# Kernel optimization log

Hardware: AMD Instinct MI355X
Metric: run time of the kernel (lower is better)

## Reference

```python
import jax, jax.numpy as jnp
import numpy as np

KROT = 8
DIM = 4096
GROUP = 128
N = 16384  # tokens (batch*seq)


def setup_inputs() -> dict:
    key = jax.random.key(0)
    k1, k2, k3 = jax.random.split(key, 3)
    x = jax.random.normal(k1, (N, DIM), dtype=jnp.float16)
    theta = (jax.random.normal(k2, (KROT, DIM // 2)) * 0.5).astype(jnp.float16)
    # pairs: per rotation layer, a permutation of [0, GROUP) tiled across groups
    # (matches torch.randperm(group_size).repeat(num_groups) in the module).
    rng = np.random.default_rng(0)
    single = np.stack([rng.permutation(GROUP) for _ in range(KROT)]).astype(np.int32)  # (KROT, GROUP)
    pairs = jnp.asarray(np.tile(single, (1, DIM // GROUP)))  # (KROT, DIM)
    channel_scales = jax.random.uniform(k3, (1, DIM), minval=0.5, maxval=1.5).astype(jnp.float16)
    return {"x": x, "pairs": pairs, "theta": theta,
            "channel_scales": channel_scales, "group_size": GROUP}


def reference(x, pairs, theta, channel_scales, group_size):
    """Pairwise Givens rotations + per-channel scaling.

    For each rotation layer k, channels are grouped into blocks of
    `group_size`; consecutive entries (pairs[k, 2i], pairs[k, 2i+1]) within a
    group define a rotated channel pair with angle theta[k, i].
    """
    krot, dim = pairs.shape
    # global channel index = group offset + within-group index from `pairs`
    offs = (jnp.arange(dim) // group_size) * group_size            # (dim,)
    gidx = pairs + offs[None, :]                                   # (krot, dim)
    a_idx = gidx[:, 0::2]                                          # (krot, dim//2)
    b_idx = gidx[:, 1::2]                                          # (krot, dim//2)

    for k in range(krot):  # krot is a small fixed constant (8)
        t = theta[k].astype(jnp.float32)
        c = jnp.cos(t).astype(x.dtype)                             # (dim//2,)
        s = jnp.sin(t).astype(x.dtype)
        xa = x[:, a_idx[k]]                                        # (N, dim//2)
        xb = x[:, b_idx[k]]
        x = x.at[:, a_idx[k]].set(c * xa - s * xb)
        x = x.at[:, b_idx[k]].set(s * xa + c * xb)
    return x * channel_scales
```

## Files before the change

### kernel.cpp

```cpp
#include <hip/hip_runtime.h>
#include <hip/hip_fp16.h>


typedef unsigned int uint32;

#define DIM    4096
#define GROUP  128
#define KROT   8
#define NGROUP 32
#define TPAD   (GROUP + 1)

__device__ __forceinline__ float bf16_to_f(unsigned short u) {
    union { uint32 i; float f; } v; v.i = ((uint32)u) << 16; return v.f;
}
__device__ __forceinline__ unsigned short f_to_bf16(float f) {
    union { float f; uint32 i; } v; v.f = f;
    uint32 x = v.i;
    return (unsigned short)((x + 0x7fffu + ((x >> 16) & 1u)) >> 16);
}
__device__ __forceinline__ float fp16_to_f(unsigned short u) {
    __half h = __ushort_as_half(u); return __half2float(h);
}
__device__ __forceinline__ unsigned short f_to_fp16(float f) {
    return __half_as_ushort(__float2half_rn(f));
}
__device__ __forceinline__ float bcast_f(float x, int lane) {
    return __uint_as_float(__builtin_amdgcn_readlane(__float_as_uint(x), lane));
}

__global__ __launch_bounds__(256) void detect_dtype(const uint32* __restrict__ scw,
                                                    int* __restrict__ flag) {
    __shared__ int cbf[256], cfp16[256];
    int b = 0, h = 0;
    for (int i = threadIdx.x; i < 2048; i += 256) {
        uint32 lo = scw[i] & 0xffffu;
        b += (lo >= 0x3F00u && lo <= 0x3FC0u);
        h += (lo >= 0x3800u && lo <= 0x3E00u);
    }
    cbf[threadIdx.x] = b; cfp16[threadIdx.x] = h;
    __syncthreads();
    for (int s = 128; s > 0; s >>= 1) {
        if (threadIdx.x < s) { cbf[threadIdx.x] += cbf[threadIdx.x + s];
                               cfp16[threadIdx.x] += cfp16[threadIdx.x + s]; }
        __syncthreads();
    }
    if (threadIdx.x == 0)
        *flag = (cbf[0] > 1024) ? 1 : ((cfp16[0] > 1024) ? 2 : 0);
}

__global__ __launch_bounds__(256) void rotate_direct(
    const void* __restrict__ Xv,
    const int*  __restrict__ pairs,
    const void* __restrict__ thetav,
    const void* __restrict__ scalesv,
    void* __restrict__ Outv,
    const int* __restrict__ flagp, int defflag)
{
    __shared__ float tile[64][TPAD];
    __shared__ float scl[GROUP];
    const int g    = blockIdx.x;
    const int row0 = blockIdx.y * 64;
    const int tid  = threadIdx.x;
    const int dt   = flagp ? *flagp : defflag;
    const int l    = tid & 63;
    const int w    = tid >> 6;
    const int pmine = w * 16 + (l & 15);

    if (tid < GROUP) {
        int c = g * GROUP + tid;
        scl[tid] = (dt == 1) ? bf16_to_f(((const unsigned short*)scalesv)[c])
                 : (dt == 2) ? fp16_to_f(((const unsigned short*)scalesv)[c])
                 : ((const float*)scalesv)[c];
    }

    int A[KROT], B[KROT]; float C[KROT], S[KROT];
    #pragma unroll
    for (int k = 0; k < KROT; ++k) {
        A[k] = pairs[k * DIM + g * GROUP + 2 * pmine];
        B[k] = pairs[k * DIM + g * GROUP + 2 * pmine + 1];
        int ti = k * (DIM / 2) + g * (GROUP / 2) + pmine;
        float th = (dt == 1) ? bf16_to_f(((const unsigned short*)thetav)[ti])
                 : (dt == 2) ? fp16_to_f(((const unsigned short*)thetav)[ti])
                 : ((const float*)thetav)[ti];
        C[k] = __builtin_cosf(th);
        S[k] = __builtin_sinf(th);
    }

    if (dt == 0) {
        const float4* X4 = (const float4*)Xv;
        for (int i = tid; i < 64 * 32; i += 256) {
            int r = i >> 5, c4 = i & 31;
            float4 v = X4[(size_t)(row0 + r) * (DIM / 4) + g * (GROUP / 4) + c4];
            tile[r][c4 * 4 + 0] = v.x; tile[r][c4 * 4 + 1] = v.y;
            tile[r][c4 * 4 + 2] = v.z; tile[r][c4 * 4 + 3] = v.w;
        }
    } else {
        const uint4* X4 = (const uint4*)Xv;
        for (int i = tid; i < 64 * 16; i += 256) {
            int r = i >> 4, c8 = i & 15;
            uint4 wv = X4[(size_t)(row0 + r) * (DIM / 8) + g * (GROUP / 8) + c8];
            uint32 ws[4] = { wv.x, wv.y, wv.z, wv.w };
            #pragma unroll
            for (int h2 = 0; h2 < 4; ++h2) {
                unsigned short lo = (unsigned short)(ws[h2] & 0xffffu);
                unsigned short hi = (unsigned short)(ws[h2] >> 16);
                tile[r][c8 * 8 + 2 * h2]     = (dt == 1) ? bf16_to_f(lo) : fp16_to_f(lo);
                tile[r][c8 * 8 + 2 * h2 + 1] = (dt == 1) ? bf16_to_f(hi) : fp16_to_f(hi);
            }
        }
    }
    __syncthreads();

    #pragma unroll
    for (int k = 0; k < KROT; ++k) {
        #pragma unroll
        for (int pp = 0; pp < 16; ++pp) {
            int   a = __builtin_amdgcn_readlane(A[k], pp);
            int   b = __builtin_amdgcn_readlane(B[k], pp);
            float c = bcast_f(C[k], pp);
            float s = bcast_f(S[k], pp);
            float xa = tile[l][a], xb = tile[l][b];
            tile[l][a] = c * xa - s * xb;
            tile[l][b] = s * xa + c * xb;
        }
        __syncthreads();
    }

    if (dt == 0) {
        float4* O4 = (float4*)Outv;
        for (int i = tid; i < 64 * 32; i += 256) {
            int r = i >> 5, c4 = i & 31;
            float4 v;
            v.x = tile[r][c4 * 4 + 0] * scl[c4 * 4 + 0];
            v.y = tile[r][c4 * 4 + 1] * scl[c4 * 4 + 1];
            v.z = tile[r][c4 * 4 + 2] * scl[c4 * 4 + 2];
            v.w = tile[r][c4 * 4 + 3] * scl[c4 * 4 + 3];
            O4[(size_t)(row0 + r) * (DIM / 4) + g * (GROUP / 4) + c4] = v;
        }
    } else {
        uint4* O4 = (uint4*)Outv;
        for (int i = tid; i < 64 * 16; i += 256) {
            int r = i >> 4, c8 = i & 15;
            uint32 ws[4];
            #pragma unroll
            for (int h2 = 0; h2 < 4; ++h2) {
                float lo = tile[r][c8 * 8 + 2 * h2]     * scl[c8 * 8 + 2 * h2];
                float hi = tile[r][c8 * 8 + 2 * h2 + 1] * scl[c8 * 8 + 2 * h2 + 1];
                unsigned short ulo = (dt == 1) ? f_to_bf16(lo) : f_to_fp16(lo);
                unsigned short uhi = (dt == 1) ? f_to_bf16(hi) : f_to_fp16(hi);
                ws[h2] = (uint32)ulo | ((uint32)uhi << 16);
            }
            uint4 wv; wv.x = ws[0]; wv.y = ws[1]; wv.z = ws[2]; wv.w = ws[3];
            O4[(size_t)(row0 + r) * (DIM / 8) + g * (GROUP / 8) + c8] = wv;
        }
    }
}

extern "C" void kernel_launch(void* const* d_in, const int* in_sizes, int n_in,
                              void* d_out, int out_size, void* d_ws, size_t ws_size,
                              hipStream_t stream) {
    const void* x      = d_in[0];
    const int*  pairs  = (const int*)d_in[1];
    const void* theta  = d_in[2];
    const void* scales = d_in[3];

    const int N = in_sizes[0] / DIM;
    const int nrowtiles = N / 64;

    int* flag = nullptr;
    if (d_ws != nullptr && ws_size >= sizeof(int)) {
        flag = (int*)d_ws;
        detect_dtype<<<1, 256, 0, stream>>>((const uint32*)scales, flag);
    }
    rotate_direct<<<dim3(NGROUP, nrowtiles), 256, 0, stream>>>(
        x, pairs, theta, scales, d_out, flag, 0);
}
```

Measured before the change: 481.3 us.

## Compose rotations into per-group matrices and apply via MFMA GEMM

Adds a kernel that folds the eight Givens rotation layers and the channel scaling into one dense 128x128 matrix per channel group, stored in the workspace. A second kernel then multiplies each 64-row input tile by that matrix with fp16/bf16 MFMA instructions, using XOR-swizzled LDS, in place of the serial per-pair LDS read-modify-write loop. This trades a few extra FLOPs and a matrix-composition prologue for much shorter dependent LDS chains. Rounding changes because the rotations are fused and the composed matrix is stored in half precision. The new path only runs when the workspace is large enough.

```diff
diff --git a/kernel.cpp b/kernel.cpp
--- a/kernel.cpp
+++ b/kernel.cpp
@@ -3,6 +3,7 @@
 
 
 typedef unsigned int uint32;
+typedef unsigned short ushort;
 
 #define DIM    4096
 #define GROUP  128
@@ -10,18 +11,22 @@
 #define NGROUP 32
 #define TPAD   (GROUP + 1)
 
-__device__ __forceinline__ float bf16_to_f(unsigned short u) {
+typedef float    f32x4 __attribute__((ext_vector_type(4)));
+typedef _Float16 f16x8 __attribute__((ext_vector_type(8)));
+typedef short    s16x8 __attribute__((ext_vector_type(8)));
+
+__device__ __forceinline__ float bf16_to_f(ushort u) {
     union { uint32 i; float f; } v; v.i = ((uint32)u) << 16; return v.f;
 }
-__device__ __forceinline__ unsigned short f_to_bf16(float f) {
+__device__ __forceinline__ ushort f_to_bf16(float f) {
     union { float f; uint32 i; } v; v.f = f;
     uint32 x = v.i;
-    return (unsigned short)((x + 0x7fffu + ((x >> 16) & 1u)) >> 16);
-}
-__device__ __forceinline__ float fp16_to_f(unsigned short u) {
+    return (ushort)((x + 0x7fffu + ((x >> 16) & 1u)) >> 16);
+}
+__device__ __forceinline__ float fp16_to_f(ushort u) {
     __half h = __ushort_as_half(u); return __half2float(h);
 }
-__device__ __forceinline__ unsigned short f_to_fp16(float f) {
+__device__ __forceinline__ ushort f_to_fp16(float f) {
     return __half_as_ushort(__float2half_rn(f));
 }
 __device__ __forceinline__ float bcast_f(float x, int lane) {
@@ -46,6 +51,237 @@
     }
     if (threadIdx.x == 0)
         *flag = (cbf[0] > 1024) ? 1 : ((cfp16[0] > 1024) ? 2 : 0);
+}
+
+__global__ __launch_bounds__(256) void compose_M(
+    const int*  __restrict__ pairs,
+    const void* __restrict__ thetav,
+    const void* __restrict__ scalesv,
+    ushort*     __restrict__ Mt,
+    const int*  __restrict__ flagp)
+{
+    __shared__ float tile[64][TPAD];
+    const int dt = *flagp;
+    if (dt == 0) return;
+    const int g    = blockIdx.x >> 1;
+    const int half = blockIdx.x & 1;
+    const int r0   = half * 64;
+    const int tid  = threadIdx.x;
+    const int l    = tid & 63;
+    const int w    = tid >> 6;
+    const int pmine = w * 16 + (l & 15);
+
+    int A[KROT], B[KROT]; float C[KROT], S[KROT];
+    #pragma unroll
+    for (int k = 0; k < KROT; ++k) {
+        A[k] = pairs[k * DIM + g * GROUP + 2 * pmine];
+        B[k] = pairs[k * DIM + g * GROUP + 2 * pmine + 1];
+        int ti = k * (DIM / 2) + g * (GROUP / 2) + pmine;
+        float th = (dt == 1) ? bf16_to_f(((const ushort*)thetav)[ti])
+                             : fp16_to_f(((const ushort*)thetav)[ti]);
+        float c = __builtin_cosf(th), s = __builtin_sinf(th);
+        if (dt == 1) { c = bf16_to_f(f_to_bf16(c)); s = bf16_to_f(f_to_bf16(s)); }
+        else         { c = fp16_to_f(f_to_fp16(c)); s = fp16_to_f(f_to_fp16(s)); }
+        C[k] = c; S[k] = s;
+    }
+
+    for (int idx = tid; idx < 64 * GROUP; idx += 256) {
+        int r = idx >> 7, c = idx & 127;
+        tile[r][c] = (r0 + r == c) ? 1.0f : 0.0f;
+    }
+    __syncthreads();
+
+    #pragma unroll
+    for (int k = 0; k < KROT; ++k) {
+        #pragma unroll
+        for (int pp = 0; pp < 16; ++pp) {
+            int   a = __builtin_amdgcn_readlane(A[k], pp);
+            int   b = __builtin_amdgcn_readlane(B[k], pp);
+            float c = bcast_f(C[k], pp);
+            float s = bcast_f(S[k], pp);
+            float xa = tile[l][a], xb = tile[l][b];
+            tile[l][a] = c * xa - s * xb;
+            tile[l][b] = s * xa + c * xb;
+        }
+        __syncthreads();
+    }
+
+    for (int it = 0; it < 4; ++it) {
+        int idx = it * 256 + tid;
+        int j = idx >> 3, cc = idx & 7;
+        float sj = (dt == 1) ? bf16_to_f(((const ushort*)scalesv)[g * GROUP + j])
+                             : fp16_to_f(((const ushort*)scalesv)[g * GROUP + j]);
+        uint32 ws4[4];
+        #pragma unroll
+        for (int h2 = 0; h2 < 4; ++h2) {
+            float lo = tile[cc * 8 + 2 * h2][j]     * sj;
+            float hi = tile[cc * 8 + 2 * h2 + 1][j] * sj;
+            ushort ulo = (dt == 1) ? f_to_bf16(lo) : f_to_fp16(lo);
+            ushort uhi = (dt == 1) ? f_to_bf16(hi) : f_to_fp16(hi);
+            ws4[h2] = (uint32)ulo | ((uint32)uhi << 16);
+        }
+        uint4 v; v.x = ws4[0]; v.y = ws4[1]; v.z = ws4[2]; v.w = ws4[3];
+        *(uint4*)(Mt + (size_t)g * GROUP * GROUP + (size_t)j * GROUP
+                     + ((size_t)(half * 8 + cc)) * 8) = v;
+    }
+}
+
+template <int DT>
+__device__ __forceinline__ void gemm_core(const ushort* __restrict__ xs,
+                                          const ushort* __restrict__ mt,
+                                          f32x4 acc[2][4], int l, int wr, int wc)
+{
+    const int lr = l & 15, q = l >> 4;
+    union U { uint4 u; f16x8 h; s16x8 s; };
+    #pragma unroll
+    for (int kk = 0; kk < 4; ++kk) {
+        U av[2];
+        #pragma unroll
+        for (int mf = 0; mf < 2; ++mf) {
+            int r = wr * 32 + mf * 16 + lr;
+            int c = (kk * 4 + q) ^ (r & 7);
+            av[mf].u = *(const uint4*)(xs + (size_t)r * GROUP + (size_t)c * 8);
+        }
+        #pragma unroll
+        for (int nf = 0; nf < 4; ++nf) {
+            int n = wc * 64 + nf * 16 + lr;
+            int c = (kk * 4 + q) ^ (n & 7);
+            U bv; bv.u = *(const uint4*)(mt + (size_t)n * GROUP + (size_t)c * 8);
+            #pragma unroll
+            for (int mf = 0; mf < 2; ++mf) {
+                if constexpr (DT == 2)
+                    acc[mf][nf] = __builtin_amdgcn_mfma_f32_16x16x32_f16(
+                        av[mf].h, bv.h, acc[mf][nf], 0, 0, 0);
+                else
+                    acc[mf][nf] = __builtin_amdgcn_mfma_f32_16x16x32_bf16(
+                        av[mf].s, bv.s, acc[mf][nf], 0, 0, 0);
+            }
+        }
+    }
+}
+
+__global__ __launch_bounds__(256) void rotate_gemm(
+    const void* __restrict__ Xv,
+    const ushort* __restrict__ Mt,
+    void* __restrict__ Outv,
+    const int* __restrict__ flagp,
+    const int* __restrict__ pairs,
+    const void* __restrict__ thetav,
+    const void* __restrict__ scalesv)
+{
+    __shared__ union __align__(16) {
+        struct { ushort xs[64 * GROUP]; ushort mt[GROUP * GROUP]; } s;
+        ushort os[64][136];
+        struct { float tile[64][TPAD]; float scl[GROUP]; } fb;
+    } sh;
+    const int dt   = *flagp;
+    const int row0 = blockIdx.x * 64;
+    const int g    = blockIdx.y;
+    const int tid  = threadIdx.x;
+    const int l    = tid & 63;
+    const int w    = tid >> 6;
+
+    if (dt != 0) {
+        const uint4* X4 = (const uint4*)Xv;
+        #pragma unroll
+        for (int it = 0; it < 4; ++it) {
+            int i = it * 256 + tid;
+            int r = i >> 4, c = i & 15;
+            uint4 v = X4[(size_t)(row0 + r) * (DIM / 8) + g * (GROUP / 8) + c];
+            *(uint4*)(sh.s.xs + (size_t)r * GROUP + (size_t)(c ^ (r & 7)) * 8) = v;
+        }
+        const uint4* M4 = (const uint4*)(Mt + (size_t)g * GROUP * GROUP);
+        #pragma unroll
+        for (int it = 0; it < 8; ++it) {
+            int i = it * 256 + tid;
+            int n = i >> 4, c = i & 15;
+            uint4 v = M4[i];
+            *(uint4*)(sh.s.mt + (size_t)n * GROUP + (size_t)(c ^ (n & 7)) * 8) = v;
+        }
+        __syncthreads();
+
+        const int wr = w >> 1, wc = w & 1;
+        f32x4 acc[2][4];
+        #pragma unroll
+        for (int mf = 0; mf < 2; ++mf)
+            #pragma unroll
+            for (int nf = 0; nf < 4; ++nf)
+                acc[mf][nf] = (f32x4)0.0f;
+
+        if (dt == 2) gemm_core<2>(sh.s.xs, sh.s.mt, acc, l, wr, wc);
+        else         gemm_core<1>(sh.s.xs, sh.s.mt, acc, l, wr, wc);
+        __syncthreads();
+
+        const int lr = l & 15, q = l >> 4;
+        #pragma unroll
+        for (int mf = 0; mf < 2; ++mf) {
+            #pragma unroll
+            for (int nf = 0; nf < 4; ++nf) {
+                int r  = wr * 32 + mf * 16 + q * 4;
+                int cc = wc * 64 + nf * 16 + lr;
+                #pragma unroll
+                for (int j = 0; j < 4; ++j) {
+                    float vv = acc[mf][nf][j];
+                    sh.os[r + j][cc] = (dt == 1) ? f_to_bf16(vv) : f_to_fp16(vv);
+                }
+            }
+        }
+        __syncthreads();
+
+        uint4* O4 = (uint4*)Outv;
+        #pragma unroll
+        for (int it = 0; it < 2; ++it) {
+            int i = it * 256 + tid;
+            int r = i >> 3, c8 = i & 7;
+            uint4 v = *(const uint4*)(&sh.os[r][c8 * 8]);
+            O4[(size_t)(row0 + r) * (DIM / 8) + g * (GROUP / 8) + c8] = v;
+        }
+        return;
+    }
+
+    const int pmine = w * 16 + (l & 15);
+    if (tid < GROUP) sh.fb.scl[tid] = ((const float*)scalesv)[g * GROUP + tid];
+    int A[KROT], B[KROT]; float C[KROT], S[KROT];
+    #pragma unroll
+    for (int k = 0; k < KROT; ++k) {
+        A[k] = pairs[k * DIM + g * GROUP + 2 * pmine];
+        B[k] = pairs[k * DIM + g * GROUP + 2 * pmine + 1];
+        int ti = k * (DIM / 2) + g * (GROUP / 2) + pmine;
+        float th = ((const float*)thetav)[ti];
+        C[k] = __builtin_cosf(th); S[k] = __builtin_sinf(th);
+    }
+    const float4* Xf = (const float4*)Xv;
+    for (int i = tid; i < 64 * 32; i += 256) {
+        int r = i >> 5, c4 = i & 31;
+        float4 v = Xf[(size_t)(row0 + r) * (DIM / 4) + g * (GROUP / 4) + c4];
+        sh.fb.tile[r][c4 * 4 + 0] = v.x; sh.fb.tile[r][c4 * 4 + 1] = v.y;
+        sh.fb.tile[r][c4 * 4 + 2] = v.z; sh.fb.tile[r][c4 * 4 + 3] = v.w;
+    }
+    __syncthreads();
+    #pragma unroll
+    for (int k = 0; k < KROT; ++k) {
+        #pragma unroll
+        for (int pp = 0; pp < 16; ++pp) {
+            int   a = __builtin_amdgcn_readlane(A[k], pp);
+            int   b = __builtin_amdgcn_readlane(B[k], pp);
+            float c = bcast_f(C[k], pp);
+            float s = bcast_f(S[k], pp);
+            float xa = sh.fb.tile[l][a], xb = sh.fb.tile[l][b];
+            sh.fb.tile[l][a] = c * xa - s * xb;
+            sh.fb.tile[l][b] = s * xa + c * xb;
+        }
+        __syncthreads();
+    }
+    float4* Of = (float4*)Outv;
+    for (int i = tid; i < 64 * 32; i += 256) {
+        int r = i >> 5, c4 = i & 31;
+        float4 v;
+        v.x = sh.fb.tile[r][c4 * 4 + 0] * sh.fb.scl[c4 * 4 + 0];
+        v.y = sh.fb.tile[r][c4 * 4 + 1] * sh.fb.scl[c4 * 4 + 1];
+        v.z = sh.fb.tile[r][c4 * 4 + 2] * sh.fb.scl[c4 * 4 + 2];
+        v.w = sh.fb.tile[r][c4 * 4 + 3] * sh.fb.scl[c4 * 4 + 3];
+        Of[(size_t)(row0 + r) * (DIM / 4) + g * (GROUP / 4) + c4] = v;
+    }
 }
 
 __global__ __launch_bounds__(256) void rotate_direct(
@@ -68,24 +304,22 @@
 
     if (tid < GROUP) {
         int c = g * GROUP + tid;
-        scl[tid] = (dt == 1) ? bf16_to_f(((const unsigned short*)scalesv)[c])
-                 : (dt == 2) ? fp16_to_f(((const unsigned short*)scalesv)[c])
+        scl[tid] = (dt == 1) ? bf16_to_f(((const ushort*)scalesv)[c])
+                 : (dt == 2) ? fp16_to_f(((const ushort*)scalesv)[c])
                  : ((const float*)scalesv)[c];
     }
-
     int A[KROT], B[KROT]; float C[KROT], S[KROT];
     #pragma unroll
     for (int k = 0; k < KROT; ++k) {
         A[k] = pairs[k * DIM + g * GROUP + 2 * pmine];
         B[k] = pairs[k * DIM + g * GROUP + 2 * pmine + 1];
         int ti = k * (DIM / 2) + g * (GROUP / 2) + pmine;
-        float th = (dt == 1) ? bf16_to_f(((const unsigned short*)thetav)[ti])
-                 : (dt == 2) ? fp16_to_f(((const unsigned short*)thetav)[ti])
+        float th = (dt == 1) ? bf16_to_f(((const ushort*)thetav)[ti])
+                 : (dt == 2) ? fp16_to_f(((const ushort*)thetav)[ti])
                  : ((const float*)thetav)[ti];
         C[k] = __builtin_cosf(th);
         S[k] = __builtin_sinf(th);
     }
-
     if (dt == 0) {
         const float4* X4 = (const float4*)Xv;
         for (int i = tid; i < 64 * 32; i += 256) {
@@ -102,15 +336,14 @@
             uint32 ws[4] = { wv.x, wv.y, wv.z, wv.w };
             #pragma unroll
             for (int h2 = 0; h2 < 4; ++h2) {
-                unsigned short lo = (unsigned short)(ws[h2] & 0xffffu);
-                unsigned short hi = (unsigned short)(ws[h2] >> 16);
+                ushort lo = (ushort)(ws[h2] & 0xffffu);
+                ushort hi = (ushort)(ws[h2] >> 16);
                 tile[r][c8 * 8 + 2 * h2]     = (dt == 1) ? bf16_to_f(lo) : fp16_to_f(lo);
                 tile[r][c8 * 8 + 2 * h2 + 1] = (dt == 1) ? bf16_to_f(hi) : fp16_to_f(hi);
             }
         }
     }
     __syncthreads();
-
     #pragma unroll
     for (int k = 0; k < KROT; ++k) {
         #pragma unroll
@@ -125,7 +358,6 @@
         }
         __syncthreads();
     }
-
     if (dt == 0) {
         float4* O4 = (float4*)Outv;
         for (int i = tid; i < 64 * 32; i += 256) {
@@ -146,8 +378,8 @@
             for (int h2 = 0; h2 < 4; ++h2) {
                 float lo = tile[r][c8 * 8 + 2 * h2]     * scl[c8 * 8 + 2 * h2];
                 float hi = tile[r][c8 * 8 + 2 * h2 + 1] * scl[c8 * 8 + 2 * h2 + 1];
-                unsigned short ulo = (dt == 1) ? f_to_bf16(lo) : f_to_fp16(lo);
-                unsigned short uhi = (dt == 1) ? f_to_bf16(hi) : f_to_fp16(hi);
+                ushort ulo = (dt == 1) ? f_to_bf16(lo) : f_to_fp16(lo);
+                ushort uhi = (dt == 1) ? f_to_bf16(hi) : f_to_fp16(hi);
                 ws[h2] = (uint32)ulo | ((uint32)uhi << 16);
             }
             uint4 wv; wv.x = ws[0]; wv.y = ws[1]; wv.z = ws[2]; wv.w = ws[3];
@@ -164,14 +396,25 @@
     const void* theta  = d_in[2];
     const void* scales = d_in[3];
 
-    const int N = in_sizes[0] / DIM;
-    const int nrowtiles = N / 64;
-
-    int* flag = nullptr;
-    if (d_ws != nullptr && ws_size >= sizeof(int)) {
-        flag = (int*)d_ws;
+    const int N16 = in_sizes[0] / DIM;
+    const int nrowtiles = N16 / 64;
+
+    const size_t NEED = 64 + (size_t)NGROUP * GROUP * GROUP * 2;
+
+    if (d_ws != nullptr && ws_size >= NEED) {
+        int*    flag = (int*)d_ws;
+        ushort* Mt   = (ushort*)((char*)d_ws + 64);
         detect_dtype<<<1, 256, 0, stream>>>((const uint32*)scales, flag);
-    }
-    rotate_direct<<<dim3(NGROUP, nrowtiles), 256, 0, stream>>>(
-        x, pairs, theta, scales, d_out, flag, 0);
-}
+        compose_M<<<64, 256, 0, stream>>>(pairs, theta, scales, Mt, flag);
+        rotate_gemm<<<dim3(nrowtiles, NGROUP), 256, 0, stream>>>(
+            x, Mt, d_out, flag, pairs, theta, scales);
+    } else if (d_ws != nullptr && ws_size >= sizeof(int)) {
+        int* flag = (int*)d_ws;
+        detect_dtype<<<1, 256, 0, stream>>>((const uint32*)scales, flag);
+        rotate_direct<<<dim3(NGROUP, nrowtiles), 256, 0, stream>>>(
+            x, pairs, theta, scales, d_out, flag, 0);
+    } else {
+        rotate_direct<<<dim3(NGROUP, nrowtiles), 256, 0, stream>>>(
+            x, pairs, theta, scales, d_out, nullptr, 0);
+    }
+}
```

Measured after the change: 525.2 us. +9.1%, slower.
